# Performance work log

Hardware: AMD Instinct MI355X
Metric: run time of the kernel (lower is better)

The kernel has to match this reference:

```python
import jax, jax.numpy as jnp
import numpy as np

N, E, D, H = 50000, 800000, 128, 128


def _uniform_param(key, shape, fan_in):
    bound = 1.0 / np.sqrt(fan_in)
    return jax.random.uniform(key, shape, jnp.float32, -bound, bound)


def setup_inputs() -> dict:
    key = jax.random.key(0)
    ks = jax.random.split(key, 12)
    x = jax.random.normal(ks[0], (N, D), jnp.float32)
    xedge = jax.random.randint(ks[1], (2, E), 0, N, jnp.int64)
    y = jax.random.randint(ks[2], (N,), 0, 2, jnp.int32).astype(bool)
    return {
        "x": x,
        "xedge": xedge,
        "y": y,
        "pretrain": 0,
        # SAGEConv layer 1 (in=D, out=H): lin_l (with bias) applied to mean aggr, lin_r (no bias) to self
        "W1l": _uniform_param(ks[3], (D, H), D),
        "b1l": _uniform_param(ks[4], (H,), D),
        "W1r": _uniform_param(ks[5], (D, H), D),
        # SAGEConv layer 2 (in=H, out=H)
        "W2l": _uniform_param(ks[6], (H, H), H),
        "b2l": _uniform_param(ks[7], (H,), H),
        "W2r": _uniform_param(ks[8], (H, H), H),
        # Decoder weight [H, H]
        "Wdec": _uniform_param(ks[9], (H, H), H),
    }


def sage_conv(h, src, dst, Wl, bl, Wr, num_nodes):
    # gather neighbor features along edges, mean-aggregate by destination
    msgs = h[src]                                            # [E, d]
    agg = jax.ops.segment_sum(msgs, dst, num_segments=num_nodes)
    cnt = jax.ops.segment_sum(jnp.ones((src.shape[0],), h.dtype), dst,
                              num_segments=num_nodes)
    mean = agg / jnp.maximum(cnt, 1.0)[:, None]              # [N, d]
    return mean @ Wl + bl + h @ Wr                           # [N, out]


def reference(x, xedge, y, pretrain, W1l, b1l, W1r, W2l, b2l, W2r, Wdec):
    src, dst = xedge[0], xedge[1]
    n = x.shape[0]
    # Encoder: SAGE = conv1 -> relu -> (dropout: eval identity) -> conv2
    h = jax.nn.relu(sage_conv(x, src, dst, W1l, b1l, W1r, n))
    emb = sage_conv(h, src, dst, W2l, b2l, W2r, n)           # [N, H]
    # Decoder
    dx = emb @ Wdec                                          # [N, H]
    # BCEWithLogits: pos nodes target 1, neg nodes target 0, mean within each group
    ym = y.astype(dx.dtype)                                  # [N]
    n_pos = jnp.sum(ym)
    n_neg = n - n_pos
    hdim = dx.shape[1]
    sp_pos = jax.nn.softplus(-dx)   # bce(logit, 1)
    sp_neg = jax.nn.softplus(dx)    # bce(logit, 0)
    l2 = jnp.sum(sp_pos * ym[:, None]) / (jnp.maximum(n_pos, 1.0) * hdim)
    l1 = jnp.sum(sp_neg * (1.0 - ym)[:, None]) / (jnp.maximum(n_neg, 1.0) * hdim)
    return (l1 + l2, emb)
```

## Files before the change

kernel.cpp:

```cpp
#include <hip/hip_runtime.h>
#include <hip/hip_bf16.h>

#define NDIM 128
#define MROWS 32
#define BTHREADS 512
#define SCAN_CHUNK 1024

typedef __attribute__((ext_vector_type(8))) short short8;
typedef __attribute__((ext_vector_type(4))) float f32x4;

__device__ __forceinline__ float bf2f(__hip_bfloat16 v) { return __bfloat162float(v); }

__device__ __forceinline__ float ldf(const void* p, long i, int f32) {
    return f32 ? ((const float*)p)[i] : bf2f(((const __hip_bfloat16*)p)[i]);
}
__device__ __forceinline__ void stf(void* p, long i, int f32, float v) {
    if (f32) ((float*)p)[i] = v;
    else     ((__hip_bfloat16*)p)[i] = __float2bfloat16(v);
}
__device__ __forceinline__ short f2bf(float v) {
    __hip_bfloat16 h = __float2bfloat16(v);
    short s;
    __builtin_memcpy(&s, &h, 2);
    return s;
}
__device__ __forceinline__ float bflo(unsigned u) { u <<= 16; float f; __builtin_memcpy(&f, &u, 4); return f; }
__device__ __forceinline__ float bfhi(unsigned u) { u &= 0xffff0000u; float f; __builtin_memcpy(&f, &u, 4); return f; }
__device__ __forceinline__ unsigned packbf(float a, float b) {
    unsigned la = (unsigned short)f2bf(a);
    unsigned hb = (unsigned short)f2bf(b);
    return (hb << 16) | la;
}
__device__ __forceinline__ int aswz(int m, int k) {
    return m * NDIM + ((((k >> 3) ^ (m & 7)) << 3) | (k & 7));
}
__device__ __forceinline__ int wswz(int m, int p) {
    return m * 64 + ((((p >> 2) ^ (m & 7)) << 2) | (p & 3));
}

#define GLOAD(dst, sa, voff)                                              \
    asm volatile("global_load_dword %0, %1, %2"                           \
                 : "=v"(dst) : "v"(voff), "s"(sa) : "memory")


__global__ void prep_kernel(const void* __restrict__ x,
                            const void* __restrict__ W1l, const void* __restrict__ b1l,
                            const void* __restrict__ W1r, const void* __restrict__ W2l,
                            const void* __restrict__ b2l, const void* __restrict__ W2r,
                            const void* __restrict__ Wd,
                            short* __restrict__ T1l, short* __restrict__ T1r,
                            short* __restrict__ T2l, short* __restrict__ T2r,
                            short* __restrict__ Td, float* __restrict__ b1c,
                            float* __restrict__ b2c, unsigned* __restrict__ xb,
                            const int* __restrict__ xedge, int E,
                            int* __restrict__ cnt, int N,
                            int* __restrict__ flags) {
    __shared__ int s_se, s_sc;
    const int t = threadIdx.x;
    if (t == 0) { s_se = 1; s_sc = 0; }
    __syncthreads();
    {
        for (int i = t; i < 512; i += 256)
            if (xedge[2 * i + 1] != 0) s_se = 0;
        const unsigned short* xh = (const unsigned short*)x;
        int c = 0;
        for (int i = t; i < 1024; i += 256) {
            int ex = (xh[2 * i] >> 7) & 0xFF;
            if (ex >= 100 && ex <= 150) c++;
        }
        atomicAdd(&s_sc, c);
    }
    __syncthreads();
    const int e64 = s_se;
    const int wf = (s_sc < 900) ? 1 : 0;
    if (blockIdx.x == 0 && t == 0) {
        flags[0] = e64;
        flags[2] = wf;
    }
    const long idx = (long)blockIdx.x * 256 + t;
    if (idx < E) {
        int d = e64 ? xedge[2 * (E + idx)] : xedge[E + idx];
        atomicAdd(&cnt[d], 1);
    }
    if (idx < NDIM * NDIM) {
        int k = (int)(idx >> 7), n = (int)(idx & 127);
        int o = n * NDIM + k;
        T1l[o] = f2bf(ldf(W1l, idx, wf));
        T1r[o] = f2bf(ldf(W1r, idx, wf));
        T2l[o] = f2bf(ldf(W2l, idx, wf));
        T2r[o] = f2bf(ldf(W2r, idx, wf));
        Td [o] = f2bf(ldf(Wd , idx, wf));
        if (idx < NDIM) { b1c[idx] = ldf(b1l, idx, wf); b2c[idx] = ldf(b2l, idx, wf); }
    }
    if (wf) {
        const long np = (long)N * 64;
        const long stride = (long)gridDim.x * 256;
        for (long pidx = idx; pidx < np; pidx += stride) {
            float2 v = ((const float2*)x)[pidx];
            xb[pidx] = packbf(v.x, v.y);
        }
    }
}


__global__ void scan_partial(const int* __restrict__ cnt, int* __restrict__ bsum, int N) {
    __shared__ int red[256];
    const int t = threadIdx.x;
    const long base = (long)blockIdx.x * SCAN_CHUNK + (long)t * 4;
    int s = 0;
#pragma unroll
    for (int i = 0; i < 4; ++i) { long idx = base + i; if (idx < N) s += cnt[idx]; }
    red[t] = s;
    __syncthreads();
    for (int off = 128; off >= 1; off >>= 1) {
        if (t < off) red[t] += red[t + off];
        __syncthreads();
    }
    if (t == 0) bsum[blockIdx.x] = red[0];
}

__global__ void scan_bsums(const int* __restrict__ bsum, int* __restrict__ boff,
                           int B, int* __restrict__ rowptr, int N,
                           const unsigned int* __restrict__ yw,
                           int* __restrict__ flags) {
    __shared__ int part[1024];
    const int t = threadIdx.x;
    __shared__ int s_sy;
    if (t == 0) s_sy = 0;
    __syncthreads();
    if (t < 256) {
        for (int i = t; i < 1024; i += 256)
            if (yw[i] > 1u) s_sy = 1;
    }
    int v = (t < B) ? bsum[t] : 0;
    part[t] = v;
    __syncthreads();
    for (int off = 1; off < 1024; off <<= 1) {
        int u = (t >= off) ? part[t - off] : 0;
        __syncthreads();
        part[t] += u;
        __syncthreads();
    }
    if (t < B) boff[t] = part[t] - v;
    if (t == 1023) rowptr[N] = part[1023];
    if (t == 0) flags[1] = s_sy;
}

__global__ void scan_scatter(int* __restrict__ cnt, const int* __restrict__ boff,
                             int* __restrict__ rowptr, int N) {
    __shared__ int tsum[256];
    const int t = threadIdx.x;
    const long base = (long)blockIdx.x * SCAN_CHUNK + (long)t * 4;
    int loc[4];
    int s = 0;
#pragma unroll
    for (int i = 0; i < 4; ++i) {
        long idx = base + i;
        int c = (idx < N) ? cnt[idx] : 0;
        loc[i] = s;
        s += c;
    }
    tsum[t] = s;
    __syncthreads();
    for (int off = 1; off < 256; off <<= 1) {
        int u = (t >= off) ? tsum[t - off] : 0;
        __syncthreads();
        tsum[t] += u;
        __syncthreads();
    }
    const int texcl = tsum[t] - s;
    const int b0 = boff[blockIdx.x];
#pragma unroll
    for (int i = 0; i < 4; ++i) {
        long idx = base + i;
        if (idx < N) {
            int v = b0 + texcl + loc[i];
            rowptr[idx] = v;
            cnt[idx] = v;
        }
    }
}

__global__ void fill_kernel(const int* __restrict__ xedge, int E,
                            const int* __restrict__ flags,
                            int* __restrict__ cur, int* __restrict__ col) {
    int e = blockIdx.x * blockDim.x + threadIdx.x;
    if (e >= E) return;
    const int e64 = flags[0];
    int s = e64 ? xedge[2 * e] : xedge[e];
    int d = e64 ? xedge[2 * (E + e)] : xedge[E + e];
    int p = atomicAdd(&cur[d], 1);
    col[p] = s;
}


template <bool RELU, int OUTMODE>
__global__ __launch_bounds__(BTHREADS, 2)
void layer_mfma(const unsigned* __restrict__ Xb, const unsigned* __restrict__ Xraw,
                const int* __restrict__ rowptr,
                const int* __restrict__ col, const short* __restrict__ WlT,
                const float* __restrict__ biasc, const short* __restrict__ WrT,
                const short* __restrict__ WdT, const void* __restrict__ yv,
                const int* __restrict__ flags, void* __restrict__ outp,
                float* __restrict__ accum, int* __restrict__ npos, int N) {
    __shared__ short AS[2 * MROWS * NDIM];
    __shared__ int ylds[MROWS];
    __shared__ float redm[8][2];
    short* Ms = AS;
    short* Ss = AS + MROWS * NDIM;
    unsigned* Msw = (unsigned*)Ms;
    unsigned* Ssw = (unsigned*)Ss;
    const int t = threadIdx.x;
    const int n0 = blockIdx.x * MROWS;
    const int wf = flags[2];
    const unsigned* __restrict__ X = wf ? Xb : Xraw;

    if (OUTMODE == 1 && t < MROWS) {
        const int yb = flags[1];
        int n = n0 + t;
        int yn = -1;
        if (n < N)
            yn = yb ? (int)((const unsigned char*)yv)[n]
                    : (((const int*)yv)[n] != 0 ? 1 : 0);
        ylds[t] = yn;
    }

    {
        const int p = t & 63;
        const unsigned voff = (unsigned)(p * 4);
        const unsigned long long Xb64 = (unsigned long long)(uintptr_t)X;
        const int g = __builtin_amdgcn_readfirstlane(t >> 6);
        int r = g;
        int b = 0, e = 0;
        {
            int n = n0 + r;
            if (n < N) {
                b = __builtin_amdgcn_readfirstlane(rowptr[n]);
                e = __builtin_amdgcn_readfirstlane(rowptr[n + 1]);
            }
        }
        for (int it = 0; it < 4; ++it, r += 8) {
            const int n = n0 + r;
            const int deg = e - b;
            const int* colb = col + b;
            int cs[32];
            if (deg > 0) {
#pragma unroll
                for (int j = 0; j < 8; ++j) {
                    int c = __builtin_amdgcn_readfirstlane(colb[j]);
                    cs[j] = ((unsigned)c >= (unsigned)N) ? 0 : c;
                }
            }
            if (deg > 8) {
#pragma unroll
                for (int j = 8; j < 16; ++j) {
                    int c = __builtin_amdgcn_readfirstlane(colb[j]);
                    cs[j] = ((unsigned)c >= (unsigned)N) ? 0 : c;
                }
            }
            if (deg > 16) {
#pragma unroll
                for (int j = 16; j < 24; ++j) {
                    int c = __builtin_amdgcn_readfirstlane(colb[j]);
                    cs[j] = ((unsigned)c >= (unsigned)N) ? 0 : c;
                }
            }
            if (deg > 24) {
#pragma unroll
                for (int j = 24; j < 32; ++j) {
                    int c = __builtin_amdgcn_readfirstlane(colb[j]);
                    cs[j] = ((unsigned)c >= (unsigned)N) ? 0 : c;
                }
            }
            unsigned u[32];
            unsigned su = 0;
            if (n < N) {
                unsigned long long sa = Xb64 + ((unsigned long long)(unsigned)n << 8);
                GLOAD(su, sa, voff);
            }
            if (deg > 0) {
#pragma unroll
                for (int j = 0; j < 8; ++j) {
                    unsigned long long sa = Xb64 + ((unsigned long long)(unsigned)cs[j] << 8);
                    GLOAD(u[j], sa, voff);
                }
            }
            if (deg > 8) {
#pragma unroll
                for (int j = 8; j < 16; ++j) {
                    unsigned long long sa = Xb64 + ((unsigned long long)(unsigned)cs[j] << 8);
                    GLOAD(u[j], sa, voff);
                }
            }
            if (deg > 16) {
#pragma unroll
                for (int j = 16; j < 24; ++j) {
                    unsigned long long sa = Xb64 + ((unsigned long long)(unsigned)cs[j] << 8);
                    GLOAD(u[j], sa, voff);
                }
            }
            if (deg > 24) {
#pragma unroll
                for (int j = 24; j < 32; ++j) {
                    unsigned long long sa = Xb64 + ((unsigned long long)(unsigned)cs[j] << 8);
                    GLOAD(u[j], sa, voff);
                }
            }
            int bn = 0, en = 0;
            if (it < 3) {
                int nn = n0 + r + 8;
                if (nn < N) {
                    bn = __builtin_amdgcn_readfirstlane(rowptr[nn]);
                    en = __builtin_amdgcn_readfirstlane(rowptr[nn + 1]);
                }
            }
            asm volatile("s_waitcnt vmcnt(0)" ::: "memory");
            __builtin_amdgcn_sched_barrier(0);
            if (n < N) asm volatile("" : "+v"(su));
            if (deg > 0) {
#pragma unroll
                for (int j = 0; j < 8; ++j) asm volatile("" : "+v"(u[j]));
            }
            if (deg > 8) {
#pragma unroll
                for (int j = 8; j < 16; ++j) asm volatile("" : "+v"(u[j]));
            }
            if (deg > 16) {
#pragma unroll
                for (int j = 16; j < 24; ++j) asm volatile("" : "+v"(u[j]));
            }
            if (deg > 24) {
#pragma unroll
                for (int j = 24; j < 32; ++j) asm volatile("" : "+v"(u[j]));
            }
            float m0 = 0.f, m1 = 0.f;
            if (deg > 0) {
                float p0 = 0.f, p1 = 0.f, p2 = 0.f, p3 = 0.f;
                float q0 = 0.f, q1 = 0.f, q2 = 0.f, q3 = 0.f;
#pragma unroll
                for (int j = 0; j < 32; j += 4) {
                    if (j + 0 < deg) { p0 += bflo(u[j]);     q0 += bfhi(u[j]); }
                    if (j + 1 < deg) { p1 += bflo(u[j + 1]); q1 += bfhi(u[j + 1]); }
                    if (j + 2 < deg) { p2 += bflo(u[j + 2]); q2 += bfhi(u[j + 2]); }
                    if (j + 3 < deg) { p3 += bflo(u[j + 3]); q3 += bfhi(u[j + 3]); }
                }
                m0 = (p0 + p1) + (p2 + p3);
                m1 = (q0 + q1) + (q2 + q3);
                for (int i = b + 32; i < e; ++i) {
                    int c = __builtin_amdgcn_readfirstlane(col[i]);
                    unsigned uu = X[(long)c * 64 + p];
                    m0 += bflo(uu);
                    m1 += bfhi(uu);
                }
                float inv = 1.f / (float)deg;
                m0 *= inv; m1 *= inv;
            }
            int wi = wswz(r, p);
            Msw[wi] = packbf(m0, m1);
            Ssw[wi] = su;
            b = bn; e = en;
        }
    }
    __syncthreads();
    const int l = t & 63, w = t >> 6;
    const int quad = l >> 4, l15 = l & 15;
    const int wcol = w * 16;
    f32x4 acc[2] = {};
    for (int k0 = 0; k0 < NDIM; k0 += 32) {
        const int kc = k0 + quad * 8;
        short8 ams[2], ass[2], bl, br;
#pragma unroll
        for (int rt = 0; rt < 2; ++rt) {
            int m = rt * 16 + l15;
            ams[rt] = *(const short8*)&Ms[aswz(m, kc)];
            ass[rt] = *(const short8*)&Ss[aswz(m, kc)];
        }
        {
            int n = wcol + l15;
            bl = *(const short8*)&WlT[n * NDIM + kc];
            br = *(const short8*)&WrT[n * NDIM + kc];
        }
#pragma unroll
        for (int rt = 0; rt < 2; ++rt) {
            acc[rt] = __builtin_amdgcn_mfma_f32_16x16x32_bf16(
                ams[rt], bl, acc[rt], 0, 0, 0);
            acc[rt] = __builtin_amdgcn_mfma_f32_16x16x32_bf16(
                ass[rt], br, acc[rt], 0, 0, 0);
        }
    }
    __syncthreads();

    if (OUTMODE == 0) {
        {
            int cg = wcol + l15;
            float bv = biasc[cg];
#pragma unroll
            for (int rt = 0; rt < 2; ++rt)
#pragma unroll
                for (int reg = 0; reg < 4; ++reg) {
                    int row = rt * 16 + quad * 4 + reg;
                    float v = acc[rt][reg] + bv;
                    if (RELU) v = fmaxf(v, 0.f);
                    Ms[row * NDIM + cg] = f2bf(v);
                }
        }
        __syncthreads();
        unsigned* ob = (unsigned*)outp;
        for (int idx = t; idx < MROWS * 64; idx += BTHREADS) {
            int r = idx >> 6;
            if (n0 + r < N) ob[(long)n0 * 64 + idx] = Msw[idx];
        }
    } else {
        {
            int cg = wcol + l15;
            float bv = biasc[cg];
#pragma unroll
            for (int rt = 0; rt < 2; ++rt)
#pragma unroll
                for (int reg = 0; reg < 4; ++reg) {
                    int row = rt * 16 + quad * 4 + reg;
                    float v = acc[rt][reg] + bv;
                    Ms[aswz(row, cg)] = f2bf(v);
                    int n = n0 + row;
                    if (n < N) {
                        if (wf) ((float*)outp)[1 + (long)n * NDIM + cg] = v;
                        else ((__hip_bfloat16*)outp)[1 + (long)n * NDIM + cg] =
                                 __float2bfloat16(v);
                    }
                }
        }
        __syncthreads();
        f32x4 acc2[2] = {};
        for (int k0 = 0; k0 < NDIM; k0 += 32) {
            const int kc = k0 + quad * 8;
            short8 a[2], bwd;
#pragma unroll
            for (int rt = 0; rt < 2; ++rt)
                a[rt] = *(const short8*)&Ms[aswz(rt * 16 + l15, kc)];
            bwd = *(const short8*)&WdT[(wcol + l15) * NDIM + kc];
#pragma unroll
            for (int rt = 0; rt < 2; ++rt)
                acc2[rt] = __builtin_amdgcn_mfma_f32_16x16x32_bf16(
                    a[rt], bwd, acc2[rt], 0, 0, 0);
        }
        float lpos = 0.f, lneg = 0.f;
#pragma unroll
        for (int rt = 0; rt < 2; ++rt)
#pragma unroll
            for (int reg = 0; reg < 4; ++reg) {
                int row = rt * 16 + quad * 4 + reg;
                int yn = ylds[row];
                if (yn >= 0) {
                    float z = acc2[rt][reg];
                    float L = log1pf(expf(-fabsf(z)));
                    if (yn) lpos += fmaxf(-z, 0.f) + L;
                    else    lneg += fmaxf(z, 0.f) + L;
                }
            }
#pragma unroll
        for (int off = 32; off >= 1; off >>= 1) {
            lpos += __shfl_down(lpos, off, 64);
            lneg += __shfl_down(lneg, off, 64);
        }
        if (l == 0) { redm[w][0] = lpos; redm[w][1] = lneg; }
        __syncthreads();
        if (t == 0) {
            float sp = 0.f, sn = 0.f;
#pragma unroll
            for (int i = 0; i < 8; ++i) { sp += redm[i][0]; sn += redm[i][1]; }
            atomicAdd(&accum[0], sp);
            atomicAdd(&accum[1], sn);
            int c = 0;
            for (int i = 0; i < MROWS; ++i) if (ylds[i] > 0) c++;
            if (c) atomicAdd(npos, c);
        }
    }
}

__global__ void finalize_kernel(const float* __restrict__ accum, const int* __restrict__ npos,
                                const int* __restrict__ flags, void* __restrict__ out, int N) {
    float np_ = (float)(*npos);
    float nn_ = (float)N - np_;
    float l2 = accum[0] / (fmaxf(np_, 1.f) * 128.f);
    float l1 = accum[1] / (fmaxf(nn_, 1.f) * 128.f);
    stf(out, 0, flags[2], l1 + l2);
}


extern "C" void kernel_launch(void* const* d_in, const int* in_sizes, int n_in,
                              void* d_out, int out_size, void* d_ws, size_t ws_size,
                              hipStream_t stream) {
    const void* x    = d_in[0];
    const int* xedge = (const int*)d_in[1];
    const void* y    = d_in[2];
    const void* W1l  = d_in[4];
    const void* b1l  = d_in[5];
    const void* W1r  = d_in[6];
    const void* W2l  = d_in[7];
    const void* b2l  = d_in[8];
    const void* W2r  = d_in[9];
    const void* Wdec = d_in[10];

    const int N = in_sizes[0] / NDIM;
    const int E = in_sizes[1] / 2;

    char* ws = (char*)d_ws;
    size_t off = 0;
    auto alloc = [&](size_t bytes) -> void* {
        void* p = ws + off;
        off = (off + bytes + 255) & ~(size_t)255;
        return p;
    };
    int*   flags  = (int*)alloc(64);
    float* accum  = (float*)alloc(64);
    int*   npos   = (int*)alloc(64);
    int*   bsum   = (int*)alloc(1024 * 4);
    int*   boff   = (int*)alloc(1024 * 4);
    int*   cnt    = (int*)alloc((size_t)N * 4);
    int*   rowptr = (int*)alloc((size_t)(N + 1) * 4);
    int*   col    = (int*)alloc((size_t)E * 4);
    unsigned* xb  = (unsigned*)alloc((size_t)N * 64 * 4);
    unsigned* hbuf = (unsigned*)alloc((size_t)N * 64 * 4);
    short* T1l = (short*)alloc(NDIM * NDIM * 2);
    short* T1r = (short*)alloc(NDIM * NDIM * 2);
    short* T2l = (short*)alloc(NDIM * NDIM * 2);
    short* T2r = (short*)alloc(NDIM * NDIM * 2);
    short* Td  = (short*)alloc(NDIM * NDIM * 2);
    float* b1c = (float*)alloc(NDIM * 4);
    float* b2c = (float*)alloc(NDIM * 4);

    hipMemsetAsync(cnt, 0, (size_t)N * 4, stream);
    hipMemsetAsync(accum, 0, 64, stream);
    hipMemsetAsync(npos, 0, 64, stream);

    const long prep_items = (E > NDIM * NDIM) ? E : NDIM * NDIM;
    prep_kernel<<<(int)((prep_items + 255) / 256), 256, 0, stream>>>(
        x, W1l, b1l, W1r, W2l, b2l, W2r, Wdec,
        T1l, T1r, T2l, T2r, Td, b1c, b2c, xb, xedge, E, cnt, N, flags);

    const int sb = (N + SCAN_CHUNK - 1) / SCAN_CHUNK;
    scan_partial<<<sb, 256, 0, stream>>>(cnt, bsum, N);
    scan_bsums<<<1, 1024, 0, stream>>>(bsum, boff, sb, rowptr, N,
                                       (const unsigned int*)y, flags);
    scan_scatter<<<sb, 256, 0, stream>>>(cnt, boff, rowptr, N);

    const int eb = (E + 255) / 256;
    fill_kernel<<<eb, 256, 0, stream>>>(xedge, E, flags, cnt, col);

    const int nbM = (N + MROWS - 1) / MROWS;
    layer_mfma<true, 0><<<nbM, BTHREADS, 0, stream>>>(
        xb, (const unsigned*)x, rowptr, col, T1l, b1c, T1r, nullptr, nullptr,
        flags, hbuf, nullptr, nullptr, N);
    layer_mfma<false, 1><<<nbM, BTHREADS, 0, stream>>>(
        hbuf, hbuf, rowptr, col, T2l, b2c, T2r, Td, y, flags,
        d_out, accum, npos, N);
    finalize_kernel<<<1, 1, 0, stream>>>(accum, npos, flags, d_out, N);
}
```

Before: 311.9 us.

## Gather neighbor rows with 16-byte loads and merge scan and memset launches

The neighbor gather in the layer kernel now has each wavefront split into four 16-lane groups. Each group fetches a different edge's row with dwordx4 loads, and the partial sums are combined with cross-lane shuffles. This replaces per-lane dword loads of one row per edge, cutting the load instruction count, and column indices are fetched once with a vector load plus shuffles instead of serial scalar loads. The separate block-sum scan kernel is removed: each scatter block reduces the preceding block sums itself, and the label-format check moves into scan_partial. The three memsets become one by moving the allocations next to each other. This adds shuffle reductions and redundant prefix work per block, and relies on the adjacent buffer layout to be correct.

```diff
diff --git a/kernel.cpp b/kernel.cpp
--- a/kernel.cpp
+++ b/kernel.cpp
@@ -8,6 +8,7 @@
 
 typedef __attribute__((ext_vector_type(8))) short short8;
 typedef __attribute__((ext_vector_type(4))) float f32x4;
+typedef unsigned uint4v __attribute__((ext_vector_type(4)));
 
 __device__ __forceinline__ float bf2f(__hip_bfloat16 v) { return __bfloat162float(v); }
 
@@ -34,12 +35,12 @@
 __device__ __forceinline__ int aswz(int m, int k) {
     return m * NDIM + ((((k >> 3) ^ (m & 7)) << 3) | (k & 7));
 }
-__device__ __forceinline__ int wswz(int m, int p) {
-    return m * 64 + ((((p >> 2) ^ (m & 7)) << 2) | (p & 3));
-}
-
-#define GLOAD(dst, sa, voff)                                              \
-    asm volatile("global_load_dword %0, %1, %2"                           \
+
+#define GLOAD4V(dst, va)                                                  \
+    asm volatile("global_load_dwordx4 %0, %1, off"                        \
+                 : "=v"(dst) : "v"(va) : "memory")
+#define GLOAD4S(dst, sa, voff)                                            \
+    asm volatile("global_load_dwordx4 %0, %1, %2"                         \
                  : "=v"(dst) : "v"(voff), "s"(sa) : "memory")
 
 
@@ -103,9 +104,20 @@
 }
 
 
-__global__ void scan_partial(const int* __restrict__ cnt, int* __restrict__ bsum, int N) {
+__global__ void scan_partial(const int* __restrict__ cnt, int* __restrict__ bsum, int N,
+                             const unsigned int* __restrict__ yw,
+                             int* __restrict__ flags) {
     __shared__ int red[256];
     const int t = threadIdx.x;
+    if (blockIdx.x == 0) {
+        __shared__ int s_sy;
+        if (t == 0) s_sy = 0;
+        __syncthreads();
+        for (int i = t; i < 1024; i += 256)
+            if (yw[i] > 1u) s_sy = 1;
+        __syncthreads();
+        if (t == 0) flags[1] = s_sy;
+    }
     const long base = (long)blockIdx.x * SCAN_CHUNK + (long)t * 4;
     int s = 0;
 #pragma unroll
@@ -119,36 +131,10 @@
     if (t == 0) bsum[blockIdx.x] = red[0];
 }
 
-__global__ void scan_bsums(const int* __restrict__ bsum, int* __restrict__ boff,
-                           int B, int* __restrict__ rowptr, int N,
-                           const unsigned int* __restrict__ yw,
-                           int* __restrict__ flags) {
-    __shared__ int part[1024];
-    const int t = threadIdx.x;
-    __shared__ int s_sy;
-    if (t == 0) s_sy = 0;
-    __syncthreads();
-    if (t < 256) {
-        for (int i = t; i < 1024; i += 256)
-            if (yw[i] > 1u) s_sy = 1;
-    }
-    int v = (t < B) ? bsum[t] : 0;
-    part[t] = v;
-    __syncthreads();
-    for (int off = 1; off < 1024; off <<= 1) {
-        int u = (t >= off) ? part[t - off] : 0;
-        __syncthreads();
-        part[t] += u;
-        __syncthreads();
-    }
-    if (t < B) boff[t] = part[t] - v;
-    if (t == 1023) rowptr[N] = part[1023];
-    if (t == 0) flags[1] = s_sy;
-}
-
-__global__ void scan_scatter(int* __restrict__ cnt, const int* __restrict__ boff,
+__global__ void scan_scatter(int* __restrict__ cnt, const int* __restrict__ bsum,
                              int* __restrict__ rowptr, int N) {
     __shared__ int tsum[256];
+    __shared__ int red[256];
     const int t = threadIdx.x;
     const long base = (long)blockIdx.x * SCAN_CHUNK + (long)t * 4;
     int loc[4];
@@ -161,6 +147,9 @@
         s += c;
     }
     tsum[t] = s;
+    int sown = 0;
+    for (int i = t; i < blockIdx.x; i += 256) sown += bsum[i];
+    red[t] = sown;
     __syncthreads();
     for (int off = 1; off < 256; off <<= 1) {
         int u = (t >= off) ? tsum[t - off] : 0;
@@ -168,8 +157,12 @@
         tsum[t] += u;
         __syncthreads();
     }
+    for (int off = 128; off >= 1; off >>= 1) {
+        if (t < off) red[t] += red[t + off];
+        __syncthreads();
+    }
+    const int b0 = red[0];
     const int texcl = tsum[t] - s;
-    const int b0 = boff[blockIdx.x];
 #pragma unroll
     for (int i = 0; i < 4; ++i) {
         long idx = base + i;
@@ -179,6 +172,7 @@
             cnt[idx] = v;
         }
     }
+    if (blockIdx.x == gridDim.x - 1 && t == 255) rowptr[N] = b0 + tsum[255];
 }
 
 __global__ void fill_kernel(const int* __restrict__ xedge, int E,
@@ -209,7 +203,8 @@
     short* Ms = AS;
     short* Ss = AS + MROWS * NDIM;
     unsigned* Msw = (unsigned*)Ms;
-    unsigned* Ssw = (unsigned*)Ss;
+    uint4v* Msw4 = (uint4v*)Ms;
+    uint4v* Ssw4 = (uint4v*)Ss;
     const int t = threadIdx.x;
     const int n0 = blockIdx.x * MROWS;
     const int wf = flags[2];
@@ -226,11 +221,14 @@
     }
 
     {
-        const int p = t & 63;
-        const unsigned voff = (unsigned)(p * 4);
+        const int l = t & 63;
+        const int g16 = l >> 4;
+        const int q = l & 15;
         const unsigned long long Xb64 = (unsigned long long)(uintptr_t)X;
-        const int g = __builtin_amdgcn_readfirstlane(t >> 6);
-        int r = g;
+        const unsigned long long base16 = Xb64 + (unsigned)(q << 4);
+        const unsigned voff16 = (unsigned)(q << 4);
+        const int wv = __builtin_amdgcn_readfirstlane(t >> 6);
+        int r = wv;
         int b = 0, e = 0;
         {
             int n = n0 + r;
@@ -242,69 +240,11 @@
         for (int it = 0; it < 4; ++it, r += 8) {
             const int n = n0 + r;
             const int deg = e - b;
-            const int* colb = col + b;
-            int cs[32];
+            int colv = 0;
             if (deg > 0) {
-#pragma unroll
-                for (int j = 0; j < 8; ++j) {
-                    int c = __builtin_amdgcn_readfirstlane(colb[j]);
-                    cs[j] = ((unsigned)c >= (unsigned)N) ? 0 : c;
-                }
-            }
-            if (deg > 8) {
-#pragma unroll
-                for (int j = 8; j < 16; ++j) {
-                    int c = __builtin_amdgcn_readfirstlane(colb[j]);
-                    cs[j] = ((unsigned)c >= (unsigned)N) ? 0 : c;
-                }
-            }
-            if (deg > 16) {
-#pragma unroll
-                for (int j = 16; j < 24; ++j) {
-                    int c = __builtin_amdgcn_readfirstlane(colb[j]);
-                    cs[j] = ((unsigned)c >= (unsigned)N) ? 0 : c;
-                }
-            }
-            if (deg > 24) {
-#pragma unroll
-                for (int j = 24; j < 32; ++j) {
-                    int c = __builtin_amdgcn_readfirstlane(colb[j]);
-                    cs[j] = ((unsigned)c >= (unsigned)N) ? 0 : c;
-                }
-            }
-            unsigned u[32];
-            unsigned su = 0;
-            if (n < N) {
-                unsigned long long sa = Xb64 + ((unsigned long long)(unsigned)n << 8);
-                GLOAD(su, sa, voff);
-            }
-            if (deg > 0) {
-#pragma unroll
-                for (int j = 0; j < 8; ++j) {
-                    unsigned long long sa = Xb64 + ((unsigned long long)(unsigned)cs[j] << 8);
-                    GLOAD(u[j], sa, voff);
-                }
-            }
-            if (deg > 8) {
-#pragma unroll
-                for (int j = 8; j < 16; ++j) {
-                    unsigned long long sa = Xb64 + ((unsigned long long)(unsigned)cs[j] << 8);
-                    GLOAD(u[j], sa, voff);
-                }
-            }
-            if (deg > 16) {
-#pragma unroll
-                for (int j = 16; j < 24; ++j) {
-                    unsigned long long sa = Xb64 + ((unsigned long long)(unsigned)cs[j] << 8);
-                    GLOAD(u[j], sa, voff);
-                }
-            }
-            if (deg > 24) {
-#pragma unroll
-                for (int j = 24; j < 32; ++j) {
-                    unsigned long long sa = Xb64 + ((unsigned long long)(unsigned)cs[j] << 8);
-                    GLOAD(u[j], sa, voff);
-                }
+                int cl = b + (l & 31);
+                if (cl >= e) cl = e - 1;
+                colv = col[cl];
             }
             int bn = 0, en = 0;
             if (it < 3) {
@@ -314,50 +254,78 @@
                     en = __builtin_amdgcn_readfirstlane(rowptr[nn + 1]);
                 }
             }
+            int c[8];
+            if (deg > 0) {
+#pragma unroll
+                for (int i = 0; i < 8; ++i) {
+                    int ci = __shfl(colv, 4 * i + g16, 64);
+                    c[i] = ((unsigned)ci >= (unsigned)N) ? 0 : ci;
+                }
+            }
+            uint4v u4[8];
+            uint4v su4 = {0, 0, 0, 0};
+            const int havesu = (n < N) && (l < 16);
+            if (havesu) {
+                unsigned long long sa = Xb64 + ((unsigned long long)(unsigned)n << 8);
+                GLOAD4S(su4, sa, voff16);
+            }
+            if (deg > 0) {
+#pragma unroll
+                for (int i = 0; i < 8; ++i) {
+                    unsigned long long va = base16 + ((unsigned long long)(unsigned)c[i] << 8);
+                    GLOAD4V(u4[i], va);
+                }
+            }
             asm volatile("s_waitcnt vmcnt(0)" ::: "memory");
             __builtin_amdgcn_sched_barrier(0);
-            if (n < N) asm volatile("" : "+v"(su));
+            if (havesu) asm volatile("" : "+v"(su4));
             if (deg > 0) {
 #pragma unroll
-                for (int j = 0; j < 8; ++j) asm volatile("" : "+v"(u[j]));
-            }
-            if (deg > 8) {
-#pragma unroll
-                for (int j = 8; j < 16; ++j) asm volatile("" : "+v"(u[j]));
-            }
-            if (deg > 16) {
-#pragma unroll
-                for (int j = 16; j < 24; ++j) asm volatile("" : "+v"(u[j]));
-            }
-            if (deg > 24) {
-#pragma unroll
-                for (int j = 24; j < 32; ++j) asm volatile("" : "+v"(u[j]));
-            }
-            float m0 = 0.f, m1 = 0.f;
+                for (int i = 0; i < 8; ++i) asm volatile("" : "+v"(u4[i]));
+            }
+            float m[8];
+#pragma unroll
+            for (int k = 0; k < 8; ++k) m[k] = 0.f;
             if (deg > 0) {
-                float p0 = 0.f, p1 = 0.f, p2 = 0.f, p3 = 0.f;
-                float q0 = 0.f, q1 = 0.f, q2 = 0.f, q3 = 0.f;
-#pragma unroll
-                for (int j = 0; j < 32; j += 4) {
-                    if (j + 0 < deg) { p0 += bflo(u[j]);     q0 += bfhi(u[j]); }
-                    if (j + 1 < deg) { p1 += bflo(u[j + 1]); q1 += bfhi(u[j + 1]); }
-                    if (j + 2 < deg) { p2 += bflo(u[j + 2]); q2 += bfhi(u[j + 2]); }
-                    if (j + 3 < deg) { p3 += bflo(u[j + 3]); q3 += bfhi(u[j + 3]); }
-                }
-                m0 = (p0 + p1) + (p2 + p3);
-                m1 = (q0 + q1) + (q2 + q3);
-                for (int i = b + 32; i < e; ++i) {
-                    int c = __builtin_amdgcn_readfirstlane(col[i]);
-                    unsigned uu = X[(long)c * 64 + p];
-                    m0 += bflo(uu);
-                    m1 += bfhi(uu);
+#pragma unroll
+                for (int i = 0; i < 8; ++i) {
+                    if (4 * i + g16 < deg) {
+#pragma unroll
+                        for (int j = 0; j < 4; ++j) {
+                            m[2 * j]     += bflo(u4[i][j]);
+                            m[2 * j + 1] += bfhi(u4[i][j]);
+                        }
+                    }
+                }
+#pragma unroll
+                for (int k = 0; k < 8; ++k) m[k] += __shfl_xor(m[k], 16, 64);
+#pragma unroll
+                for (int k = 0; k < 8; ++k) m[k] += __shfl_xor(m[k], 32, 64);
+                if (deg > 32 && l < 16) {
+                    const uint4v* X4 = (const uint4v*)X;
+                    for (int i2 = b + 32; i2 < e; ++i2) {
+                        int cc = __builtin_amdgcn_readfirstlane(col[i2]);
+                        uint4v uu = X4[(long)cc * 16 + q];
+#pragma unroll
+                        for (int j = 0; j < 4; ++j) {
+                            m[2 * j]     += bflo(uu[j]);
+                            m[2 * j + 1] += bfhi(uu[j]);
+                        }
+                    }
                 }
                 float inv = 1.f / (float)deg;
-                m0 *= inv; m1 *= inv;
-            }
-            int wi = wswz(r, p);
-            Msw[wi] = packbf(m0, m1);
-            Ssw[wi] = su;
+#pragma unroll
+                for (int k = 0; k < 8; ++k) m[k] *= inv;
+            }
+            if (l < 16) {
+                uint4v outw;
+#pragma unroll
+                for (int j = 0; j < 4; ++j)
+                    outw[j] = packbf(m[2 * j], m[2 * j + 1]);
+                int wi4 = r * 16 + (q ^ (r & 7));
+                Msw4[wi4] = outw;
+                Ssw4[wi4] = su4;
+            }
             b = bn; e = en;
         }
     }
@@ -512,11 +480,10 @@
         return p;
     };
     int*   flags  = (int*)alloc(64);
+    int*   cnt    = (int*)alloc((size_t)N * 4);
     float* accum  = (float*)alloc(64);
     int*   npos   = (int*)alloc(64);
     int*   bsum   = (int*)alloc(1024 * 4);
-    int*   boff   = (int*)alloc(1024 * 4);
-    int*   cnt    = (int*)alloc((size_t)N * 4);
     int*   rowptr = (int*)alloc((size_t)(N + 1) * 4);
     int*   col    = (int*)alloc((size_t)E * 4);
     unsigned* xb  = (unsigned*)alloc((size_t)N * 64 * 4);
@@ -529,9 +496,8 @@
     float* b1c = (float*)alloc(NDIM * 4);
     float* b2c = (float*)alloc(NDIM * 4);
 
-    hipMemsetAsync(cnt, 0, (size_t)N * 4, stream);
-    hipMemsetAsync(accum, 0, 64, stream);
-    hipMemsetAsync(npos, 0, 64, stream);
+    const size_t zlen = (((size_t)N * 4 + 255) & ~(size_t)255) + 512;
+    hipMemsetAsync(cnt, 0, zlen, stream);
 
     const long prep_items = (E > NDIM * NDIM) ? E : NDIM * NDIM;
     prep_kernel<<<(int)((prep_items + 255) / 256), 256, 0, stream>>>(
@@ -539,10 +505,8 @@
         T1l, T1r, T2l, T2r, Td, b1c, b2c, xb, xedge, E, cnt, N, flags);
 
     const int sb = (N + SCAN_CHUNK - 1) / SCAN_CHUNK;
-    scan_partial<<<sb, 256, 0, stream>>>(cnt, bsum, N);
-    scan_bsums<<<1, 1024, 0, stream>>>(bsum, boff, sb, rowptr, N,
-                                       (const unsigned int*)y, flags);
-    scan_scatter<<<sb, 256, 0, stream>>>(cnt, boff, rowptr, N);
+    scan_partial<<<sb, 256, 0, stream>>>(cnt, bsum, N, (const unsigned int*)y, flags);
+    scan_scatter<<<sb, 256, 0, stream>>>(cnt, bsum, rowptr, N);
 
     const int eb = (E + 255) / 256;
     fill_kernel<<<eb, 256, 0, stream>>>(xedge, E, flags, cnt, col);
```

Result: slower. 334.4 us (+7.2%).
